# Kernel optimization log

Hardware: AMD Instinct MI355X
Metric: run time of the kernel (lower is better)

The kernel has to match this reference:

```python
import jax, jax.numpy as jnp
import numpy as np

B, N, NFG, NFR = 512, 64, 1024, 256
OH, OW = 87, 157
POS_THRESHOLD = 0.2


def setup_inputs() -> dict:
    key = jax.random.key(0)
    ks = jax.random.split(key, 7)
    feats = jax.random.normal(ks[0], (B, N, NFG), dtype=jnp.float32)
    # boxes (x1,y1,x2,y2) in image coordinates
    boxes = jax.random.uniform(ks[1], (B, N, 4), dtype=jnp.float32)
    scale = jnp.array([OW, OH, OW, OH], dtype=jnp.float32)
    boxes = boxes * scale
    s_in = 1.0 / np.sqrt(NFG)
    W_theta = jax.random.normal(ks[2], (NFG, NFR), dtype=jnp.float32) * s_in
    b_theta = jnp.zeros((NFR,), dtype=jnp.float32)
    W_phi = jax.random.normal(ks[3], (NFG, NFR), dtype=jnp.float32) * s_in
    b_phi = jnp.zeros((NFR,), dtype=jnp.float32)
    W_gcn = jax.random.normal(ks[4], (NFG, NFG), dtype=jnp.float32) * s_in
    return {
        "graph_boxes_features": feats,
        "boxes_in_flat": boxes,
        "W_theta": W_theta,
        "b_theta": b_theta,
        "W_phi": W_phi,
        "b_phi": b_phi,
        "W_gcn": W_gcn,
    }


def reference(graph_boxes_features, boxes_in_flat, W_theta, b_theta, W_phi, b_phi, W_gcn):
    nfr = W_theta.shape[-1]
    # box centers [B,N,2]
    cx = (boxes_in_flat[..., 0] + boxes_in_flat[..., 2]) * 0.5
    cy = (boxes_in_flat[..., 1] + boxes_in_flat[..., 3]) * 0.5
    pos = jnp.stack([cx, cy], axis=-1)  # [B,N,2]
    # pairwise euclidean distances [B,N,N]
    diff = pos[:, :, None, :] - pos[:, None, :, :]
    dist = jnp.sqrt(jnp.sum(diff * diff, axis=-1))
    position_mask = dist > (POS_THRESHOLD * OW)

    theta = jnp.einsum('bnf,fr->bnr', graph_boxes_features, W_theta) + b_theta
    phi = jnp.einsum('bnf,fr->bnr', graph_boxes_features, W_phi) + b_phi
    sim = jnp.einsum('bnr,bmr->bnm', theta, phi) / jnp.sqrt(jnp.asarray(nfr, theta.dtype))
    logits = jnp.where(position_mask, -jnp.inf, sim)
    relation_graph = jax.nn.softmax(logits, axis=2)  # [B,N,N]

    agg = jnp.einsum('bnm,bmf->bnf', relation_graph, graph_boxes_features)
    out = jax.nn.relu(jnp.einsum('bnf,fg->bng', agg, W_gcn))
    return out, relation_graph
```

## Files before the change

### kernel.cpp

```cpp
#include <hip/hip_runtime.h>
#include <hip/hip_bf16.h>
#include <math.h>

#define BB   512
#define NN   64
#define NFG  1024
#define NFR  256
#define MM   (BB * NN)
#define RG_OFF 33554432L

typedef __attribute__((ext_vector_type(8))) short bf16x8;
typedef __attribute__((ext_vector_type(4))) float f32x4;
typedef __attribute__((ext_vector_type(8))) unsigned short u16x8;

__device__ inline unsigned short f2bf(float f) {
    union { float f; unsigned u; } v; v.f = f;
    unsigned u = v.u;
    return (unsigned short)((u + 0x7FFFu + ((u >> 16) & 1u)) >> 16);
}
__device__ inline float bf2f(unsigned short h) {
    union { unsigned u; float f; } v; v.u = ((unsigned)h) << 16;
    return v.f;
}

__device__ inline void gld_lds16(const unsigned short* g, unsigned short* l) {
    __builtin_amdgcn_global_load_lds((const __attribute__((address_space(1))) void*)g,
                                     (__attribute__((address_space(3))) void*)l, 16, 0, 0);
}


__global__ __launch_bounds__(256) void cast_f32_bf16(const float* __restrict__ in,
                                                     unsigned short* __restrict__ out, long n) {
    long i = ((long)blockIdx.x * 256 + threadIdx.x) * 8;
    if (i + 8 <= n) {
        f32x4 a = *(const f32x4*)(in + i);
        f32x4 b = *(const f32x4*)(in + i + 4);
        u16x8 o;
#pragma unroll
        for (int c = 0; c < 4; ++c) { o[c] = f2bf(a[c]); o[4 + c] = f2bf(b[c]); }
        *(u16x8*)(out + i) = o;
    }
}

__global__ void transpose_cast(const float* __restrict__ in, unsigned short* __restrict__ out,
                               int K, int N) {
    __shared__ float tile[32][33];
    int tx = threadIdx.x, ty = threadIdx.y;
    int k0 = blockIdx.y * 32, n0 = blockIdx.x * 32;
#pragma unroll
    for (int r = 0; r < 4; ++r)
        tile[ty + r * 8][tx] = in[(long)(k0 + ty + r * 8) * N + n0 + tx];
    __syncthreads();
#pragma unroll
    for (int r = 0; r < 4; ++r)
        out[(long)(n0 + ty + r * 8) * K + k0 + tx] = f2bf(tile[tx][ty + r * 8]);
}

__global__ void concat_bias(const float* __restrict__ bt, const float* __restrict__ bp,
                            float* __restrict__ out) {
    int i = threadIdx.x;
    out[i] = (i < 256) ? bt[i] : bp[i - 256];
}


template<int RELU, int STORE_BF16>
__global__ __launch_bounds__(256)
void gemm_bt(const unsigned short* __restrict__ A, const unsigned short* __restrict__ Bt,
             const float* __restrict__ bias, void* __restrict__ Cout,
             int M, int N, int K) {
    __shared__ __align__(16) unsigned short As[128 * 32];
    __shared__ __align__(16) unsigned short Bs[128 * 32];
    const int t    = threadIdx.x;
    const int lane = t & 63;
    const int w    = t >> 6;
    const int l15  = lane & 15;
    const int q    = lane >> 4;
    const long tileM = (long)blockIdx.x * 128;
    const long tileN = (long)blockIdx.y * 128;
    const int wm = (w & 1) * 64;
    const int wn = (w >> 1) * 64;

    f32x4 acc[4][4] = {};

    const int rS = t >> 2;
    const int cS = t & 3;
    const unsigned short* gA0 = A  + (tileM + rS) * (long)K + cS * 8;
    const unsigned short* gA1 = gA0 + 64L * K;
    const unsigned short* gB0 = Bt + (tileN + rS) * (long)K + cS * 8;
    const unsigned short* gB1 = gB0 + 64L * K;
    unsigned short* lA0 = As + (0 * 256 + w * 64) * 8;
    unsigned short* lA1 = As + (1 * 256 + w * 64) * 8;
    unsigned short* lB0 = Bs + (0 * 256 + w * 64) * 8;
    unsigned short* lB1 = Bs + (1 * 256 + w * 64) * 8;

    for (int kt = 0; kt < K; kt += 32) {
        __syncthreads();
        gld_lds16(gA0 + kt, lA0);
        gld_lds16(gA1 + kt, lA1);
        gld_lds16(gB0 + kt, lB0);
        gld_lds16(gB1 + kt, lB1);
        __syncthreads();
        bf16x8 af[4], bf[4];
#pragma unroll
        for (int mi = 0; mi < 4; ++mi)
            af[mi] = *(const bf16x8*)(As + (wm + mi * 16 + l15) * 32 + q * 8);
#pragma unroll
        for (int ni = 0; ni < 4; ++ni)
            bf[ni] = *(const bf16x8*)(Bs + (wn + ni * 16 + l15) * 32 + q * 8);
#pragma unroll
        for (int mi = 0; mi < 4; ++mi)
#pragma unroll
            for (int ni = 0; ni < 4; ++ni)
                acc[mi][ni] = __builtin_amdgcn_mfma_f32_16x16x32_bf16(af[mi], bf[ni],
                                                                      acc[mi][ni], 0, 0, 0);
    }

#pragma unroll
    for (int mi = 0; mi < 4; ++mi) {
#pragma unroll
        for (int ni = 0; ni < 4; ++ni) {
            long row0 = tileM + wm + mi * 16 + q * 4;
            long col  = tileN + wn + ni * 16 + l15;
            float bv = bias ? bias[col] : 0.f;
#pragma unroll
            for (int r = 0; r < 4; ++r) {
                float v = acc[mi][ni][r] + bv;
                if (RELU) v = fmaxf(v, 0.f);
                long idx = (row0 + r) * N + col;
                if (STORE_BF16) ((unsigned short*)Cout)[idx] = f2bf(v);
                else            ((float*)Cout)[idx] = v;
            }
        }
    }
}


__global__ __launch_bounds__(256)
void fused_softmax_agg(const unsigned short* __restrict__ thetaphi,
                       const float* __restrict__ boxes,
                       const unsigned short* __restrict__ featsb,
                       float* __restrict__ rg_out,
                       unsigned short* __restrict__ aggb) {
    __shared__ __align__(16) float sim_s[64][68];
    __shared__ __align__(16) float Pt[64][68];
    __shared__ float cxs[64], cys[64];
    const int t    = threadIdx.x;
    const int b    = blockIdx.x;
    const int lane = t & 63;
    const int w    = t >> 6;
    const int l15  = lane & 15;
    const int q    = lane >> 4;

    if (t < 64) {
        float4 bx = *(const float4*)(boxes + ((long)b * 64 + t) * 4);
        cxs[t] = (bx.x + bx.z) * 0.5f;
        cys[t] = (bx.y + bx.w) * 0.5f;
    }

    {
        f32x4 acc[4] = {};
        const unsigned short* thA = thetaphi + ((long)b * 64 + w * 16 + l15) * 512 + q * 8;
        const unsigned short* thB = thetaphi + ((long)b * 64 + l15) * 512 + 256 + q * 8;
#pragma unroll
        for (int kt = 0; kt < 256; kt += 32) {
            bf16x8 a = *(const bf16x8*)(thA + kt);
#pragma unroll
            for (int ni = 0; ni < 4; ++ni) {
                bf16x8 bb = *(const bf16x8*)(thB + (long)ni * 16 * 512 + kt);
                acc[ni] = __builtin_amdgcn_mfma_f32_16x16x32_bf16(a, bb, acc[ni], 0, 0, 0);
            }
        }
#pragma unroll
        for (int ni = 0; ni < 4; ++ni)
#pragma unroll
            for (int r = 0; r < 4; ++r)
                sim_s[w * 16 + q * 4 + r][ni * 16 + l15] = acc[ni][r] * 0.0625f;
    }
    __syncthreads();

    {
        const int i  = t >> 2;
        const int j0 = (t & 3) * 16;
        const float cxi = cxs[i], cyi = cys[i];
        const float thr = (float)(0.2 * 157.0);
        float vals[16];
        float mx = -__builtin_inff();
#pragma unroll
        for (int jj = 0; jj < 16; ++jj) {
            int j = j0 + jj;
            float dx = cxi - cxs[j];
            float dy = cyi - cys[j];
            bool msk = sqrtf(dx * dx + dy * dy) > thr;
            float s = msk ? -__builtin_inff() : sim_s[i][j];
            vals[jj] = s;
            mx = fmaxf(mx, s);
        }
        mx = fmaxf(mx, __shfl_xor(mx, 1, 64));
        mx = fmaxf(mx, __shfl_xor(mx, 2, 64));
        float sum = 0.f;
#pragma unroll
        for (int jj = 0; jj < 16; ++jj) {
            float e = (vals[jj] == -__builtin_inff()) ? 0.f : __expf(vals[jj] - mx);
            vals[jj] = e;
            sum += e;
        }
        sum += __shfl_xor(sum, 1, 64);
        sum += __shfl_xor(sum, 2, 64);
        float inv = 1.f / sum;
#pragma unroll
        for (int jj = 0; jj < 16; ++jj) {
            int j = j0 + jj;
            float p = vals[jj] * inv;
            rg_out[((long)b * 64 + i) * 64 + j] = p;
            Pt[j][i] = p;
        }
    }
    __syncthreads();

    {
        const int i0 = (t >> 4) * 4;
        const int gb = t & 15;
        const unsigned short* fB = featsb + (long)b * 64 * 1024;
        unsigned short* aB = aggb + (long)b * 64 * 1024;
#pragma unroll 1
        for (int gc = 0; gc < 8; ++gc) {
            int g = gc * 128 + gb * 8;
            float acc[4][8];
#pragma unroll
            for (int r = 0; r < 4; ++r)
#pragma unroll
                for (int c = 0; c < 8; ++c) acc[r][c] = 0.f;
#pragma unroll 4
            for (int j = 0; j < 64; ++j) {
                f32x4 p = *(const f32x4*)(&Pt[j][i0]);
                u16x8 fv = *(const u16x8*)(fB + j * 1024 + g);
                float f[8];
#pragma unroll
                for (int c = 0; c < 8; ++c) f[c] = bf2f(fv[c]);
#pragma unroll
                for (int r = 0; r < 4; ++r)
#pragma unroll
                    for (int c = 0; c < 8; ++c) acc[r][c] += p[r] * f[c];
            }
#pragma unroll
            for (int r = 0; r < 4; ++r) {
                u16x8 o;
#pragma unroll
                for (int c = 0; c < 8; ++c) o[c] = f2bf(acc[r][c]);
                *(u16x8*)(aB + (i0 + r) * 1024 + g) = o;
            }
        }
    }
}


extern "C" void kernel_launch(void* const* d_in, const int* in_sizes, int n_in,
                              void* d_out, int out_size, void* d_ws, size_t ws_size,
                              hipStream_t stream) {
    const float* feats   = (const float*)d_in[0];
    const float* boxes   = (const float*)d_in[1];
    const float* W_theta = (const float*)d_in[2];
    const float* b_theta = (const float*)d_in[3];
    const float* W_phi   = (const float*)d_in[4];
    const float* b_phi   = (const float*)d_in[5];
    const float* W_gcn   = (const float*)d_in[6];
    float* out = (float*)d_out;

    char* ws = (char*)d_ws;
    unsigned short* featsb   = (unsigned short*)(ws);
    unsigned short* thetaphi = (unsigned short*)(ws + 67108864);
    unsigned short* aggb     = (unsigned short*)(ws + 100663296);
    unsigned short* Wtp      = (unsigned short*)(ws + 167772160);
    unsigned short* Wgt      = (unsigned short*)(ws + 168820736);
    float*          bias512  = (float*)(ws + 170917888);

    cast_f32_bf16<<<16384, 256, 0, stream>>>(feats, featsb, 33554432L);
    transpose_cast<<<dim3(8, 32),  dim3(32, 8), 0, stream>>>(W_theta, Wtp,              1024, 256);
    transpose_cast<<<dim3(8, 32),  dim3(32, 8), 0, stream>>>(W_phi,   Wtp + 256 * 1024, 1024, 256);
    transpose_cast<<<dim3(32, 32), dim3(32, 8), 0, stream>>>(W_gcn,   Wgt,              1024, 1024);
    concat_bias<<<1, 512, 0, stream>>>(b_theta, b_phi, bias512);

    gemm_bt<0, 1><<<dim3(256, 4), 256, 0, stream>>>(featsb, Wtp, bias512, thetaphi,
                                                    MM, 512, 1024);
    fused_softmax_agg<<<BB, 256, 0, stream>>>(thetaphi, boxes, featsb, out + RG_OFF, aggb);
    gemm_bt<1, 0><<<dim3(256, 8), 256, 0, stream>>>(aggb, Wgt, nullptr, out,
                                                    MM, 1024, 1024);
}
```

Baseline: 502.6 us.

## Reassociate GCN matmul: compute feats@W_gcn first, then apply relation graph via MFMA

The order of the two matmuls is swapped, using (R·F)·W = R·(F·W). The large GEMM now runs on the features directly and writes H in a per-batch transposed bf16 layout. The fused softmax kernel then multiplies the bf16 probabilities by H with MFMA instructions and writes the ReLU output straight away, replacing the scalar FMA aggregation loop and the separate agg buffer. The cost is an extra bf16 rounding of H before the small matmul, and ReLU now runs after the relation product, which is mathematically equivalent.

Result: no change. 498.0 us (-0.9%).

```diff
diff --git a/kernel.cpp b/kernel.cpp
--- a/kernel.cpp
+++ b/kernel.cpp
@@ -12,15 +12,12 @@
 typedef __attribute__((ext_vector_type(8))) short bf16x8;
 typedef __attribute__((ext_vector_type(4))) float f32x4;
 typedef __attribute__((ext_vector_type(8))) unsigned short u16x8;
+typedef __attribute__((ext_vector_type(4))) unsigned short u16x4;
 
 __device__ inline unsigned short f2bf(float f) {
     union { float f; unsigned u; } v; v.f = f;
     unsigned u = v.u;
     return (unsigned short)((u + 0x7FFFu + ((u >> 16) & 1u)) >> 16);
-}
-__device__ inline float bf2f(unsigned short h) {
-    union { unsigned u; float f; } v; v.u = ((unsigned)h) << 16;
-    return v.f;
 }
 
 __device__ inline void gld_lds16(const unsigned short* g, unsigned short* l) {
@@ -63,7 +60,7 @@
 }
 
 
-template<int RELU, int STORE_BF16>
+template<int RELU, int OUT_MODE>
 __global__ __launch_bounds__(256)
 void gemm_bt(const unsigned short* __restrict__ A, const unsigned short* __restrict__ Bt,
              const float* __restrict__ bias, void* __restrict__ Cout,
@@ -122,13 +119,25 @@
             long row0 = tileM + wm + mi * 16 + q * 4;
             long col  = tileN + wn + ni * 16 + l15;
             float bv = bias ? bias[col] : 0.f;
-#pragma unroll
-            for (int r = 0; r < 4; ++r) {
-                float v = acc[mi][ni][r] + bv;
-                if (RELU) v = fmaxf(v, 0.f);
-                long idx = (row0 + r) * N + col;
-                if (STORE_BF16) ((unsigned short*)Cout)[idx] = f2bf(v);
-                else            ((float*)Cout)[idx] = v;
+            if (OUT_MODE == 2) {
+                u16x4 o;
+#pragma unroll
+                for (int r = 0; r < 4; ++r) {
+                    float v = acc[mi][ni][r] + bv;
+                    if (RELU) v = fmaxf(v, 0.f);
+                    o[r] = f2bf(v);
+                }
+                long base = (row0 >> 6) * ((long)N * 64) + col * 64 + (row0 & 63);
+                *(u16x4*)((unsigned short*)Cout + base) = o;
+            } else {
+#pragma unroll
+                for (int r = 0; r < 4; ++r) {
+                    float v = acc[mi][ni][r] + bv;
+                    if (RELU) v = fmaxf(v, 0.f);
+                    long idx = (row0 + r) * N + col;
+                    if (OUT_MODE == 1) ((unsigned short*)Cout)[idx] = f2bf(v);
+                    else               ((float*)Cout)[idx] = v;
+                }
             }
         }
     }
@@ -136,13 +145,13 @@
 
 
 __global__ __launch_bounds__(256)
-void fused_softmax_agg(const unsigned short* __restrict__ thetaphi,
+void fused_softmax_out(const unsigned short* __restrict__ thetaphi,
                        const float* __restrict__ boxes,
-                       const unsigned short* __restrict__ featsb,
+                       const unsigned short* __restrict__ Ht,
                        float* __restrict__ rg_out,
-                       unsigned short* __restrict__ aggb) {
+                       float* __restrict__ out) {
     __shared__ __align__(16) float sim_s[64][68];
-    __shared__ __align__(16) float Pt[64][68];
+    __shared__ __align__(16) unsigned short Pb[64][72];
     __shared__ float cxs[64], cys[64];
     const int t    = threadIdx.x;
     const int b    = blockIdx.x;
@@ -212,42 +221,34 @@
             int j = j0 + jj;
             float p = vals[jj] * inv;
             rg_out[((long)b * 64 + i) * 64 + j] = p;
-            Pt[j][i] = p;
+            Pb[i][j] = f2bf(p);
         }
     }
     __syncthreads();
 
     {
-        const int i0 = (t >> 4) * 4;
-        const int gb = t & 15;
-        const unsigned short* fB = featsb + (long)b * 64 * 1024;
-        unsigned short* aB = aggb + (long)b * 64 * 1024;
-#pragma unroll 1
-        for (int gc = 0; gc < 8; ++gc) {
-            int g = gc * 128 + gb * 8;
-            float acc[4][8];
-#pragma unroll
-            for (int r = 0; r < 4; ++r)
-#pragma unroll
-                for (int c = 0; c < 8; ++c) acc[r][c] = 0.f;
-#pragma unroll 4
-            for (int j = 0; j < 64; ++j) {
-                f32x4 p = *(const f32x4*)(&Pt[j][i0]);
-                u16x8 fv = *(const u16x8*)(fB + j * 1024 + g);
-                float f[8];
-#pragma unroll
-                for (int c = 0; c < 8; ++c) f[c] = bf2f(fv[c]);
+        const unsigned short* HtB = Ht + (long)b * 65536;
+        float* outB = out + (long)b * 65536;
+        bf16x8 af[4][2];
+#pragma unroll
+        for (int mi = 0; mi < 4; ++mi)
+#pragma unroll
+            for (int kk = 0; kk < 2; ++kk)
+                af[mi][kk] = *(const bf16x8*)(&Pb[mi * 16 + l15][kk * 32 + q * 8]);
+#pragma unroll 2
+        for (int nt = 0; nt < 16; ++nt) {
+            const int g0 = w * 256 + nt * 16;
+            const unsigned short* hp = HtB + (long)(g0 + l15) * 64 + q * 8;
+            bf16x8 b0 = *(const bf16x8*)(hp);
+            bf16x8 b1 = *(const bf16x8*)(hp + 32);
+#pragma unroll
+            for (int mi = 0; mi < 4; ++mi) {
+                f32x4 acc = {};
+                acc = __builtin_amdgcn_mfma_f32_16x16x32_bf16(af[mi][0], b0, acc, 0, 0, 0);
+                acc = __builtin_amdgcn_mfma_f32_16x16x32_bf16(af[mi][1], b1, acc, 0, 0, 0);
 #pragma unroll
                 for (int r = 0; r < 4; ++r)
-#pragma unroll
-                    for (int c = 0; c < 8; ++c) acc[r][c] += p[r] * f[c];
-            }
-#pragma unroll
-            for (int r = 0; r < 4; ++r) {
-                u16x8 o;
-#pragma unroll
-                for (int c = 0; c < 8; ++c) o[c] = f2bf(acc[r][c]);
-                *(u16x8*)(aB + (i0 + r) * 1024 + g) = o;
+                    outB[(long)(mi * 16 + q * 4 + r) * 1024 + g0 + l15] = fmaxf(acc[r], 0.f);
             }
         }
     }
@@ -269,7 +270,7 @@
     char* ws = (char*)d_ws;
     unsigned short* featsb   = (unsigned short*)(ws);
     unsigned short* thetaphi = (unsigned short*)(ws + 67108864);
-    unsigned short* aggb     = (unsigned short*)(ws + 100663296);
+    unsigned short* Ht       = (unsigned short*)(ws + 100663296);
     unsigned short* Wtp      = (unsigned short*)(ws + 167772160);
     unsigned short* Wgt      = (unsigned short*)(ws + 168820736);
     float*          bias512  = (float*)(ws + 170917888);
@@ -282,7 +283,7 @@
 
     gemm_bt<0, 1><<<dim3(256, 4), 256, 0, stream>>>(featsb, Wtp, bias512, thetaphi,
                                                     MM, 512, 1024);
-    fused_softmax_agg<<<BB, 256, 0, stream>>>(thetaphi, boxes, featsb, out + RG_OFF, aggb);
-    gemm_bt<1, 0><<<dim3(256, 8), 256, 0, stream>>>(aggb, Wgt, nullptr, out,
+    gemm_bt<0, 2><<<dim3(256, 8), 256, 0, stream>>>(featsb, Wgt, nullptr, Ht,
                                                     MM, 1024, 1024);
-}
+    fused_softmax_out<<<BB, 256, 0, stream>>>(thetaphi, boxes, Ht, out + RG_OFF, out);
+}
```
